# Kernel optimization log

Measured on AMD Instinct MI355X. Metric: run time of the kernel, lower is better.

Reference implementation:

```python
import math
import jax, jax.numpy as jnp
import numpy as np

EMB = 1024
HEADS = 16
HD = EMB // HEADS  # 64
MAXPOS = 1024
BATCH = 4
SEQ = 1024


def get_rope_cache(dim, max_pos, theta=10000.0):
    # NOTE: faithfully reproduces the (i - 1) quirk of the source (not the standard i)
    i = jnp.arange(dim // 2, dtype=jnp.float32)
    theta_i = theta ** (-2.0 * (i - 1.0) / dim)
    pos = jnp.arange(max_pos, dtype=jnp.float32)[:, None]
    th = pos * theta_i  # [max_pos, dim//2]
    return jnp.stack([jnp.cos(th), jnp.sin(th)], axis=-1)  # [max_pos, dim//2, 2]


def apply_rope(x, rope_cache):
    # x: [B, H, S, hd]. Source casts pairs to float16 before the complex multiply,
    # then the complex32*complex64 product promotes back to float32 -> emulate via
    # an fp16 round-trip on x, with the rotation itself done in fp32.
    B, H, S, hd = x.shape
    rc = rope_cache[:S]  # [S, hd//2, 2]
    xp = x.reshape(B, H, S, hd // 2, 2).astype(jnp.float16).astype(jnp.float32)
    a, b = xp[..., 0], xp[..., 1]
    cos, sin = rc[..., 0], rc[..., 1]
    rot = jnp.stack([a * cos - b * sin, a * sin + b * cos], axis=-1)
    return rot.reshape(B, H, S, hd)


def setup_inputs() -> dict:
    key = jax.random.key(0)
    ks = jax.random.split(key, 5)
    std = math.sqrt(2.0 / (EMB + EMB))
    x = jax.random.normal(ks[0], (BATCH, SEQ, EMB), dtype=jnp.float32)
    padding_mask = jnp.ones((BATCH, SEQ), dtype=jnp.float32)
    Wq = jax.random.normal(ks[1], (EMB, EMB), dtype=jnp.float32) * std
    Wk = jax.random.normal(ks[2], (EMB, EMB), dtype=jnp.float32) * std
    Wv = jax.random.normal(ks[3], (EMB, EMB), dtype=jnp.float32) * std
    Wo = jax.random.normal(ks[4], (EMB, EMB), dtype=jnp.float32) * std
    rope_cache = get_rope_cache(HD, MAXPOS)
    return {"x": x, "padding_mask": padding_mask, "Wq": Wq, "Wk": Wk,
            "Wv": Wv, "Wo": Wo, "rope_cache": rope_cache}


def reference(x, padding_mask, Wq, Wk, Wv, Wo, rope_cache):
    B, S, E = x.shape

    def heads(t):  # [B,S,E] -> [B,H,S,hd]
        return t.reshape(B, S, HEADS, HD).transpose(0, 2, 1, 3)

    q = heads(x @ Wq.T)
    k = heads(x @ Wk.T)
    v = heads(x @ Wv.T)
    q = apply_rope(q, rope_cache)
    k = apply_rope(k, rope_cache)

    scores = jnp.einsum('bhqd,bhkd->bhqk', q, k)  # [B,H,S,S]
    causal = jnp.tril(jnp.ones((S, S), jnp.float32))
    mask = (causal[None, :, :] * padding_mask[:, None, :])[:, None]  # [B,1,S,S]
    scores = jnp.where(mask == 0, jnp.float32(-1e9), scores) / math.sqrt(HD)
    weights = jax.nn.softmax(scores, axis=-1)

    out = jnp.einsum('bhqk,bhkd->bhqd', weights, v)  # [B,H,S,hd]
    # Faithful to source: transpose(-2,-1) then .view(B,S,-1) scrambles head_dim/seq
    out = out.transpose(0, 1, 3, 2).reshape(B, S, E)
    return out @ Wo.T
```

## Files before the change

kernel.cpp:

```cpp
#include <hip/hip_runtime.h>

#define SEQ   1024
#define HEADS 16
#define HD    64
#define BATCH 4
#define EMB   1024

typedef __attribute__((ext_vector_type(8))) short  short8;
typedef __attribute__((ext_vector_type(4))) float  floatx4;

__device__ __forceinline__ unsigned short f2bf(float f) {
    unsigned u = __builtin_bit_cast(unsigned, f);
    u += 0x7FFF + ((u >> 16) & 1);
    return (unsigned short)(u >> 16);
}

__device__ __forceinline__ void g2l16(const void* g, void* l) {
    __builtin_amdgcn_global_load_lds((const __attribute__((address_space(1))) unsigned int*)g,
                                     (__attribute__((address_space(3))) unsigned int*)l,
                                     16, 0, 0);
}

__device__ __forceinline__ short8 ldsfrag(const unsigned short* base, int row, int cq) {
    int ch = cq ^ (row & 7);
    return *(const short8*)(base + row * 64 + ch * 8);
}

__global__ __launch_bounds__(256) void cvt_kernel(
    const float* __restrict__ x,  const float* __restrict__ wq,
    const float* __restrict__ wk, const float* __restrict__ wv,
    const float* __restrict__ wo,
    unsigned short* __restrict__ xb, unsigned short* __restrict__ wqkvP,
    unsigned short* __restrict__ woP) {
    int blk = blockIdx.x;
    int tid = threadIdx.x;
    if (blk < 4096) {
        size_t i = (size_t)blk * 1024 + tid * 4;
        float4 v = *(const float4*)(x + i);
        ushort4 o;
        o.x = f2bf(v.x); o.y = f2bf(v.y); o.z = f2bf(v.z); o.w = f2bf(v.w);
        *(ushort4*)(xb + i) = o;
        return;
    }
    int pblk = blk - 4096;
    const float* src; unsigned short* dst; int n0t, kt;
    if (pblk < 384) {
        n0t = pblk >> 4; kt = pblk & 15;
        int which = n0t >> 3;
        src = (which == 0) ? wq : (which == 1) ? wk : wv;
        src += (size_t)(n0t & 7) * 128 * 1024;
        dst = wqkvP + (size_t)pblk * 8192;
    } else {
        int p2 = pblk - 384;
        n0t = p2 >> 4; kt = p2 & 15;
        src = wo + (size_t)n0t * 128 * 1024;
        dst = woP + (size_t)p2 * 8192;
    }
#pragma unroll
    for (int s = 0; s < 4; s++) {
        int w    = tid * 4 + s;
        int ks   = w >> 9, jj = (w >> 6) & 7, lane = w & 63;
        int row  = jj * 16 + (lane & 15);
        int col  = kt * 64 + ks * 32 + (lane >> 4) * 8;
        const float* sp = src + (size_t)row * 1024 + col;
        float4 v0 = *(const float4*)sp;
        float4 v1 = *(const float4*)(sp + 4);
        ushort4 o0, o1;
        o0.x = f2bf(v0.x); o0.y = f2bf(v0.y); o0.z = f2bf(v0.z); o0.w = f2bf(v0.w);
        o1.x = f2bf(v1.x); o1.y = f2bf(v1.y); o1.z = f2bf(v1.z); o1.w = f2bf(v1.w);
        *(ushort4*)(dst + (size_t)w * 8)     = o0;
        *(ushort4*)(dst + (size_t)w * 8 + 4) = o1;
    }
}

__global__ __launch_bounds__(256) void gemm_qkv(
    const unsigned short* __restrict__ A, const unsigned short* __restrict__ Wp,
    unsigned short* __restrict__ outQ, unsigned short* __restrict__ outK,
    unsigned short* __restrict__ outV, const float* __restrict__ rc,
    int M, int N, int K) {
    __shared__ unsigned short As[2][128 * 64];
    const int tid  = threadIdx.x;
    const int lane = tid & 63;
    const int wid  = tid >> 6;
    const int l15  = lane & 15, quad = lane >> 4;
    const int wm   = (wid & 1) * 64, wn = (wid >> 1) * 64;
    const int nbx  = gridDim.x;
    const int cpx  = (nbx * gridDim.y) >> 3;
    const int bid  = blockIdx.y * nbx + blockIdx.x;
    const int virt = (bid & 7) * cpx + (bid >> 3);
    const int n0t  = virt % nbx;
    const int m0   = (virt / nbx) * 128, n0 = n0t * 128;
    const int boff = tid * 16;

    floatx4 acc[4][4] = {};
    const char* Ab = (const char*)A;
    const size_t rstride = (size_t)K * 2;
    const unsigned short* wpb = Wp + ((size_t)(wn >> 4) * 64 + lane) * 8;

    auto stageA = [&](int bufi, int k0) {
#pragma unroll
        for (int c = 0; c < 4; c++) {
            int o = c * 4096 + boff;
            int row = o >> 7;
            int sw  = ((o >> 4) & 7) ^ (row & 7);
            g2l16(Ab + (size_t)(m0 + row) * rstride + (size_t)k0 * 2 + sw * 16,
                  (char*)As[bufi] + o);
        }
    };

    stageA(0, 0);
    __syncthreads();

    int cur = 0;
    for (int k0 = 0; k0 < K; k0 += 64) {
        const int kt = k0 >> 6;
        const unsigned short* wp = wpb + (size_t)(n0t * 16 + kt) * 8192;
        short8 b8[2][4];
#pragma unroll
        for (int ks = 0; ks < 2; ks++)
#pragma unroll
            for (int j = 0; j < 4; j++)
                b8[ks][j] = *(const short8*)(wp + (ks * 512 + j * 64) * 8);
        __builtin_amdgcn_sched_barrier(0);
        if (k0 + 64 < K) stageA(cur ^ 1, k0 + 64);

        const unsigned short* Ac = As[cur];
#pragma unroll
        for (int ks = 0; ks < 2; ks++) {
            short8 a[4];
#pragma unroll
            for (int i = 0; i < 4; i++) a[i] = ldsfrag(Ac, wm + i * 16 + l15, ks * 4 + quad);
#pragma unroll
            for (int i = 0; i < 4; i++)
#pragma unroll
                for (int j = 0; j < 4; j++)
                    acc[i][j] = __builtin_amdgcn_mfma_f32_16x16x32_bf16(a[i], b8[ks][j], acc[i][j], 0, 0, 0);
        }
        asm volatile("s_waitcnt vmcnt(0)" ::: "memory");
        __syncthreads();
        cur ^= 1;
    }

    const int which = n0 >> 10;
#pragma unroll
    for (int i = 0; i < 4; i++) {
#pragma unroll
        for (int r = 0; r < 4; r++) {
            int m = m0 + wm + i * 16 + quad * 4 + r;
            int bb = m >> 10, s = m & 1023;
#pragma unroll
            for (int j = 0; j < 4; j++) {
                int n = n0 + wn + j * 16 + l15;
                float v = acc[i][j][r];
                int nr = n & 1023, h = nr >> 6, d = nr & 63;
                if (which < 2) {
                    float vp = __shfl_xor(v, 1);
                    float2 cs = *(const float2*)&rc[(size_t)s * 64 + (d & ~1)];
                    v = (l15 & 1) ? (vp * cs.y + v * cs.x) : (v * cs.x - vp * cs.y);
                    unsigned short* dst = (which == 0) ? outQ : outK;
                    dst[(((size_t)bb * HEADS + h) * SEQ + s) * HD + d] = f2bf(v);
                } else {
                    outV[(((size_t)bb * HEADS + h) * HD + d) * SEQ + s] = f2bf(v);
                }
            }
        }
    }
}

__global__ __launch_bounds__(256) void gemm_proj64(
    const unsigned short* __restrict__ A, const unsigned short* __restrict__ Wp,
    float* __restrict__ out, int M, int N, int K) {
    __shared__ unsigned short As[2][64 * 64];
    const int tid  = threadIdx.x;
    const int lane = tid & 63;
    const int wid  = tid >> 6;
    const int l15  = lane & 15, quad = lane >> 4;
    const int wm   = (wid & 1) * 32, wn = (wid >> 1) * 64;
    const int n0t  = blockIdx.x;
    const int m0   = blockIdx.y * 64, n0 = n0t * 128;
    const int boff = tid * 16;

    floatx4 acc[2][4] = {};
    const char* Ab = (const char*)A;
    const size_t rstride = (size_t)K * 2;
    const unsigned short* wpb = Wp + ((size_t)(wn >> 4) * 64 + lane) * 8;

    auto stageA = [&](int bufi, int k0) {
#pragma unroll
        for (int c = 0; c < 2; c++) {
            int o = c * 4096 + boff;
            int row = o >> 7;
            int sw  = ((o >> 4) & 7) ^ (row & 7);
            g2l16(Ab + (size_t)(m0 + row) * rstride + (size_t)k0 * 2 + sw * 16,
                  (char*)As[bufi] + o);
        }
    };

    stageA(0, 0);
    __syncthreads();

    int cur = 0;
    for (int k0 = 0; k0 < K; k0 += 64) {
        const int kt = k0 >> 6;
        const unsigned short* wp = wpb + (size_t)(n0t * 16 + kt) * 8192;
        short8 b8[2][4];
#pragma unroll
        for (int ks = 0; ks < 2; ks++)
#pragma unroll
            for (int j = 0; j < 4; j++)
                b8[ks][j] = *(const short8*)(wp + (ks * 512 + j * 64) * 8);
        __builtin_amdgcn_sched_barrier(0);
        if (k0 + 64 < K) stageA(cur ^ 1, k0 + 64);

        const unsigned short* Ac = As[cur];
#pragma unroll
        for (int ks = 0; ks < 2; ks++) {
            short8 a[2];
#pragma unroll
            for (int i = 0; i < 2; i++) a[i] = ldsfrag(Ac, wm + i * 16 + l15, ks * 4 + quad);
#pragma unroll
            for (int i = 0; i < 2; i++)
#pragma unroll
                for (int j = 0; j < 4; j++)
                    acc[i][j] = __builtin_amdgcn_mfma_f32_16x16x32_bf16(a[i], b8[ks][j], acc[i][j], 0, 0, 0);
        }
        asm volatile("s_waitcnt vmcnt(0)" ::: "memory");
        __syncthreads();
        cur ^= 1;
    }

#pragma unroll
    for (int i = 0; i < 2; i++) {
#pragma unroll
        for (int r = 0; r < 4; r++) {
            int m = m0 + wm + i * 16 + quad * 4 + r;
#pragma unroll
            for (int j = 0; j < 4; j++) {
                int n = n0 + wn + j * 16 + l15;
                out[(size_t)m * N + n] = acc[i][j][r];
            }
        }
    }
}

__global__ __launch_bounds__(256) void attn_kernel(
    const unsigned short* __restrict__ Qb, const unsigned short* __restrict__ Kb,
    const unsigned short* __restrict__ VTb, const float* __restrict__ pm,
    unsigned short* __restrict__ Tb) {
    __shared__ unsigned short Ks[2][64 * 64];
    __shared__ unsigned short Vs[2][64 * 64];
    const int tid  = threadIdx.x;
    const int lane = tid & 63, wid = tid >> 6;
    const int l15  = lane & 15, quad = lane >> 4;
    const int bh   = blockIdx.x, b = bh >> 4;
    const int q0   = (15 - blockIdx.y) * 64;
    const int qw   = q0 + wid * 16;
    const int q    = qw + l15;
    const unsigned short* Qh  = Qb  + (size_t)bh * SEQ * HD;
    const unsigned short* Kh  = Kb  + (size_t)bh * SEQ * HD;
    const unsigned short* VTh = VTb + (size_t)bh * HD * SEQ;
    unsigned short*       Th  = Tb  + (size_t)bh * HD * SEQ;
    const float* pmb = pm + b * SEQ;
    const float SCL2 = 0.125f * 1.44269504088896340736f;

    short8 qf0 = *(const short8*)&Qh[(size_t)q * HD + quad * 8];
    short8 qf1 = *(const short8*)&Qh[(size_t)q * HD + 32 + quad * 8];

    floatx4 ot[4] = {};
    float l_lane = 0.f;
    const int boff = tid * 16;
    const int srcA = l15 + ((quad & 1) << 5);
    const int srcB = srcA + 16;
    const bool hi  = (quad >> 1) & 1;

    auto stageKV = [&](int bufi, int kvc) {
        const char* kg = (const char*)(Kh + (size_t)kvc * HD);
        const char* vg = (const char*)(VTh + kvc);
#pragma unroll
        for (int c = 0; c < 2; c++) {
            int o = c * 4096 + boff;
            int row = o >> 7;
            int sw  = ((o >> 4) & 7) ^ (row & 7);
            g2l16(kg + (size_t)row * 128 + sw * 16, (char*)Ks[bufi] + o);
            g2l16(vg + (size_t)row * (SEQ * 2) + sw * 16, (char*)Vs[bufi] + o);
        }
    };

    stageKV(0, 0);
    __syncthreads();

    int cur = 0;
    for (int kvc = 0; kvc <= q0; kvc += 64) {
        if (kvc + 64 <= q0) stageKV(cur ^ 1, kvc + 64);

        const unsigned short* Kc = Ks[cur];
        const unsigned short* Vc = Vs[cur];
        const bool diag = (kvc + 63 > qw);
        floatx4 sc[4];
#pragma unroll
        for (int st = 0; st < 4; st++) {
            short8 ka0 = ldsfrag(Kc, st * 16 + l15, quad);
            short8 ka1 = ldsfrag(Kc, st * 16 + l15, 4 + quad);
            floatx4 z = {0.f, 0.f, 0.f, 0.f};
            z = __builtin_amdgcn_mfma_f32_16x16x32_bf16(ka0, qf0, z, 0, 0, 0);
            z = __builtin_amdgcn_mfma_f32_16x16x32_bf16(ka1, qf1, z, 0, 0, 0);
            sc[st] = z;
        }
        unsigned w0[4], w1[4];
#pragma unroll
        for (int st = 0; st < 4; st++) {
            int kvbase = kvc + st * 16 + quad * 4;
            float4 pmv = *(const float4*)&pmb[kvbase];
            float p[4];
#pragma unroll
            for (int r = 0; r < 4; r++) {
                float e = exp2f(sc[st][r] * SCL2) * (((&pmv.x)[r] != 0.f) ? 1.f : 0.f);
                if (diag && (kvbase + r > q)) e = 0.f;
                l_lane += e;
                p[r] = e;
            }
            w0[st] = (unsigned)f2bf(p[0]) | ((unsigned)f2bf(p[1]) << 16);
            w1[st] = (unsigned)f2bf(p[2]) | ((unsigned)f2bf(p[3]) << 16);
        }
        unsigned a0 = __shfl(w0[0], srcA), a1 = __shfl(w0[1], srcA);
        unsigned b0 = __shfl(w1[0], srcA), b1 = __shfl(w1[1], srcA);
        unsigned c0 = __shfl(w0[0], srcB), c1 = __shfl(w0[1], srcB);
        unsigned d0 = __shfl(w1[0], srcB), d1 = __shfl(w1[1], srcB);
        uint4 f0 = { hi ? a1 : a0, hi ? b1 : b0, hi ? c1 : c0, hi ? d1 : d0 };
        short8 pf0 = __builtin_bit_cast(short8, f0);
        a0 = __shfl(w0[2], srcA); a1 = __shfl(w0[3], srcA);
        b0 = __shfl(w1[2], srcA); b1 = __shfl(w1[3], srcA);
        c0 = __shfl(w0[2], srcB); c1 = __shfl(w0[3], srcB);
        d0 = __shfl(w1[2], srcB); d1 = __shfl(w1[3], srcB);
        uint4 f1 = { hi ? a1 : a0, hi ? b1 : b0, hi ? c1 : c0, hi ? d1 : d0 };
        short8 pf1 = __builtin_bit_cast(short8, f1);

#pragma unroll
        for (int jt = 0; jt < 4; jt++) {
            short8 v0 = ldsfrag(Vc, jt * 16 + l15, quad);
            short8 v1 = ldsfrag(Vc, jt * 16 + l15, 4 + quad);
            ot[jt] = __builtin_amdgcn_mfma_f32_16x16x32_bf16(v0, pf0, ot[jt], 0, 0, 0);
            ot[jt] = __builtin_amdgcn_mfma_f32_16x16x32_bf16(v1, pf1, ot[jt], 0, 0, 0);
        }

        asm volatile("s_waitcnt vmcnt(0)" ::: "memory");
        __syncthreads();
        cur ^= 1;
    }

    float l = l_lane;
    l += __shfl_xor(l, 16);
    l += __shfl_xor(l, 32);
    float inv = 1.0f / l;
#pragma unroll
    for (int jt = 0; jt < 4; jt++)
#pragma unroll
        for (int r = 0; r < 4; r++)
            Th[(size_t)(jt * 16 + quad * 4 + r) * SEQ + q] = f2bf(ot[jt][r] * inv);
}

extern "C" void kernel_launch(void* const* d_in, const int* in_sizes, int n_in,
                              void* d_out, int out_size, void* d_ws, size_t ws_size,
                              hipStream_t stream) {
    const float* x  = (const float*)d_in[0];
    const float* pm = (const float*)d_in[1];
    const float* Wq = (const float*)d_in[2];
    const float* Wk = (const float*)d_in[3];
    const float* Wv = (const float*)d_in[4];
    const float* Wo = (const float*)d_in[5];
    const float* rc = (const float*)d_in[6];

    char* base = (char*)d_ws;
    unsigned short* xb    = (unsigned short*)(base);
    unsigned short* wqkvP = (unsigned short*)(base + (8u  << 20));
    unsigned short* woP   = (unsigned short*)(base + (14u << 20));
    unsigned short* Qb    = (unsigned short*)(base + (16u << 20));
    unsigned short* Kb    = (unsigned short*)(base + (24u << 20));
    unsigned short* VTb   = (unsigned short*)(base + (32u << 20));
    unsigned short* Tb    = (unsigned short*)(base + (40u << 20));

    cvt_kernel<<<4608, 256, 0, stream>>>(x, Wq, Wk, Wv, Wo, xb, wqkvP, woP);
    gemm_qkv<<<dim3(24, 32), 256, 0, stream>>>(xb, wqkvP, Qb, Kb, VTb,
                                               rc, 4096, 3072, 1024);
    attn_kernel<<<dim3(64, 16), 256, 0, stream>>>(Qb, Kb, VTb, pm, Tb);
    gemm_proj64<<<dim3(8, 64), 256, 0, stream>>>(Tb, woP, (float*)d_out, 4096, 1024, 1024);
}
```

Before: 194.1 us.

## Software-pipeline QKV GEMM B-fragment loads and stage Wo through LDS

The QKV GEMM loop is unrolled by two with ping-pong registers for the packed weight fragments, so the next tile's B loads and A staging are issued before the current MFMAs. Partial vmcnt waits replace the full drain. The output projection stops using the pre-packed fragment layout: Wo is converted to plain row-major bf16 and streamed into a second swizzled LDS buffer alongside A. This trades the packing work and direct global fragment loads for more LDS traffic and shared-memory use. The cvt grid grows to cover Wo as a flat elementwise conversion.

```diff
diff --git a/kernel.cpp b/kernel.cpp
--- a/kernel.cpp
+++ b/kernel.cpp
@@ -31,7 +31,7 @@
     const float* __restrict__ wk, const float* __restrict__ wv,
     const float* __restrict__ wo,
     unsigned short* __restrict__ xb, unsigned short* __restrict__ wqkvP,
-    unsigned short* __restrict__ woP) {
+    unsigned short* __restrict__ wob) {
     int blk = blockIdx.x;
     int tid = threadIdx.x;
     if (blk < 4096) {
@@ -42,35 +42,36 @@
         *(ushort4*)(xb + i) = o;
         return;
     }
-    int pblk = blk - 4096;
-    const float* src; unsigned short* dst; int n0t, kt;
-    if (pblk < 384) {
-        n0t = pblk >> 4; kt = pblk & 15;
+    if (blk < 4480) {
+        int pblk = blk - 4096;
+        int n0t = pblk >> 4, kt = pblk & 15;
         int which = n0t >> 3;
-        src = (which == 0) ? wq : (which == 1) ? wk : wv;
+        const float* src = (which == 0) ? wq : (which == 1) ? wk : wv;
         src += (size_t)(n0t & 7) * 128 * 1024;
-        dst = wqkvP + (size_t)pblk * 8192;
-    } else {
-        int p2 = pblk - 384;
-        n0t = p2 >> 4; kt = p2 & 15;
-        src = wo + (size_t)n0t * 128 * 1024;
-        dst = woP + (size_t)p2 * 8192;
-    }
-#pragma unroll
-    for (int s = 0; s < 4; s++) {
-        int w    = tid * 4 + s;
-        int ks   = w >> 9, jj = (w >> 6) & 7, lane = w & 63;
-        int row  = jj * 16 + (lane & 15);
-        int col  = kt * 64 + ks * 32 + (lane >> 4) * 8;
-        const float* sp = src + (size_t)row * 1024 + col;
-        float4 v0 = *(const float4*)sp;
-        float4 v1 = *(const float4*)(sp + 4);
-        ushort4 o0, o1;
-        o0.x = f2bf(v0.x); o0.y = f2bf(v0.y); o0.z = f2bf(v0.z); o0.w = f2bf(v0.w);
-        o1.x = f2bf(v1.x); o1.y = f2bf(v1.y); o1.z = f2bf(v1.z); o1.w = f2bf(v1.w);
-        *(ushort4*)(dst + (size_t)w * 8)     = o0;
-        *(ushort4*)(dst + (size_t)w * 8 + 4) = o1;
-    }
+        unsigned short* dst = wqkvP + (size_t)pblk * 8192;
+#pragma unroll
+        for (int s = 0; s < 4; s++) {
+            int w    = tid * 4 + s;
+            int ks   = w >> 9, jj = (w >> 6) & 7, lane = w & 63;
+            int row  = jj * 16 + (lane & 15);
+            int col  = kt * 64 + ks * 32 + (lane >> 4) * 8;
+            const float* sp = src + (size_t)row * 1024 + col;
+            float4 v0 = *(const float4*)sp;
+            float4 v1 = *(const float4*)(sp + 4);
+            ushort4 o0, o1;
+            o0.x = f2bf(v0.x); o0.y = f2bf(v0.y); o0.z = f2bf(v0.z); o0.w = f2bf(v0.w);
+            o1.x = f2bf(v1.x); o1.y = f2bf(v1.y); o1.z = f2bf(v1.z); o1.w = f2bf(v1.w);
+            *(ushort4*)(dst + (size_t)w * 8)     = o0;
+            *(ushort4*)(dst + (size_t)w * 8 + 4) = o1;
+        }
+        return;
+    }
+    int rel = blk - 4480;
+    size_t i = (size_t)rel * 1024 + tid * 4;
+    float4 v = *(const float4*)(wo + i);
+    ushort4 o;
+    o.x = f2bf(v.x); o.y = f2bf(v.y); o.z = f2bf(v.z); o.w = f2bf(v.w);
+    *(ushort4*)(wob + i) = o;
 }
 
 __global__ __launch_bounds__(256) void gemm_qkv(
@@ -97,34 +98,25 @@
     const size_t rstride = (size_t)K * 2;
     const unsigned short* wpb = Wp + ((size_t)(wn >> 4) * 64 + lane) * 8;
 
-    auto stageA = [&](int bufi, int k0) {
+    auto stageA = [&](int bufi, int kt) {
 #pragma unroll
         for (int c = 0; c < 4; c++) {
             int o = c * 4096 + boff;
             int row = o >> 7;
             int sw  = ((o >> 4) & 7) ^ (row & 7);
-            g2l16(Ab + (size_t)(m0 + row) * rstride + (size_t)k0 * 2 + sw * 16,
+            g2l16(Ab + (size_t)(m0 + row) * rstride + (size_t)(kt << 6) * 2 + sw * 16,
                   (char*)As[bufi] + o);
         }
     };
-
-    stageA(0, 0);
-    __syncthreads();
-
-    int cur = 0;
-    for (int k0 = 0; k0 < K; k0 += 64) {
-        const int kt = k0 >> 6;
+    auto loadB = [&](short8 (&b)[2][4], int kt) {
         const unsigned short* wp = wpb + (size_t)(n0t * 16 + kt) * 8192;
-        short8 b8[2][4];
 #pragma unroll
         for (int ks = 0; ks < 2; ks++)
 #pragma unroll
             for (int j = 0; j < 4; j++)
-                b8[ks][j] = *(const short8*)(wp + (ks * 512 + j * 64) * 8);
-        __builtin_amdgcn_sched_barrier(0);
-        if (k0 + 64 < K) stageA(cur ^ 1, k0 + 64);
-
-        const unsigned short* Ac = As[cur];
+                b[ks][j] = *(const short8*)(wp + (ks * 512 + j * 64) * 8);
+    };
+    auto mfmaStep = [&](const unsigned short* Ac, short8 (&b)[2][4]) {
 #pragma unroll
         for (int ks = 0; ks < 2; ks++) {
             short8 a[4];
@@ -134,11 +126,32 @@
             for (int i = 0; i < 4; i++)
 #pragma unroll
                 for (int j = 0; j < 4; j++)
-                    acc[i][j] = __builtin_amdgcn_mfma_f32_16x16x32_bf16(a[i], b8[ks][j], acc[i][j], 0, 0, 0);
-        }
-        asm volatile("s_waitcnt vmcnt(0)" ::: "memory");
-        __syncthreads();
-        cur ^= 1;
+                    acc[i][j] = __builtin_amdgcn_mfma_f32_16x16x32_bf16(a[i], b[ks][j], acc[i][j], 0, 0, 0);
+        }
+    };
+
+    short8 bA[2][4], bB[2][4];
+    stageA(0, 0);
+    loadB(bA, 0);
+    asm volatile("s_waitcnt vmcnt(8)" ::: "memory");
+    __builtin_amdgcn_sched_barrier(0);
+    __builtin_amdgcn_s_barrier();
+
+    for (int kt = 0; kt < 16; kt += 2) {
+        if (kt + 1 < 16) { stageA(1, kt + 1); loadB(bB, kt + 1); }
+        __builtin_amdgcn_sched_barrier(0);
+        mfmaStep(As[0], bA);
+        asm volatile("s_waitcnt vmcnt(8) lgkmcnt(0)" ::: "memory");
+        __builtin_amdgcn_sched_barrier(0);
+        __builtin_amdgcn_s_barrier();
+        if (kt + 2 < 16) { stageA(0, kt + 2); loadB(bA, kt + 2); }
+        __builtin_amdgcn_sched_barrier(0);
+        mfmaStep(As[1], bB);
+        if (kt + 2 < 16) {
+            asm volatile("s_waitcnt vmcnt(8) lgkmcnt(0)" ::: "memory");
+            __builtin_amdgcn_sched_barrier(0);
+            __builtin_amdgcn_s_barrier();
+        }
     }
 
     const int which = n0 >> 10;
@@ -168,24 +181,24 @@
 }
 
 __global__ __launch_bounds__(256) void gemm_proj64(
-    const unsigned short* __restrict__ A, const unsigned short* __restrict__ Wp,
+    const unsigned short* __restrict__ A, const unsigned short* __restrict__ W,
     float* __restrict__ out, int M, int N, int K) {
     __shared__ unsigned short As[2][64 * 64];
+    __shared__ unsigned short Bs[2][128 * 64];
     const int tid  = threadIdx.x;
     const int lane = tid & 63;
     const int wid  = tid >> 6;
     const int l15  = lane & 15, quad = lane >> 4;
     const int wm   = (wid & 1) * 32, wn = (wid >> 1) * 64;
-    const int n0t  = blockIdx.x;
-    const int m0   = blockIdx.y * 64, n0 = n0t * 128;
+    const int m0   = blockIdx.y * 64, n0 = blockIdx.x * 128;
     const int boff = tid * 16;
 
     floatx4 acc[2][4] = {};
     const char* Ab = (const char*)A;
+    const char* Wb = (const char*)W;
     const size_t rstride = (size_t)K * 2;
-    const unsigned short* wpb = Wp + ((size_t)(wn >> 4) * 64 + lane) * 8;
-
-    auto stageA = [&](int bufi, int k0) {
+
+    auto stageStep = [&](int bufi, int k0) {
 #pragma unroll
         for (int c = 0; c < 2; c++) {
             int o = c * 4096 + boff;
@@ -194,36 +207,39 @@
             g2l16(Ab + (size_t)(m0 + row) * rstride + (size_t)k0 * 2 + sw * 16,
                   (char*)As[bufi] + o);
         }
+#pragma unroll
+        for (int c = 0; c < 4; c++) {
+            int o = c * 4096 + boff;
+            int row = o >> 7;
+            int sw  = ((o >> 4) & 7) ^ (row & 7);
+            g2l16(Wb + (size_t)(n0 + row) * rstride + (size_t)k0 * 2 + sw * 16,
+                  (char*)Bs[bufi] + o);
+        }
     };
 
-    stageA(0, 0);
+    stageStep(0, 0);
     __syncthreads();
 
     int cur = 0;
     for (int k0 = 0; k0 < K; k0 += 64) {
-        const int kt = k0 >> 6;
-        const unsigned short* wp = wpb + (size_t)(n0t * 16 + kt) * 8192;
-        short8 b8[2][4];
-#pragma unroll
-        for (int ks = 0; ks < 2; ks++)
-#pragma unroll
-            for (int j = 0; j < 4; j++)
-                b8[ks][j] = *(const short8*)(wp + (ks * 512 + j * 64) * 8);
-        __builtin_amdgcn_sched_barrier(0);
-        if (k0 + 64 < K) stageA(cur ^ 1, k0 + 64);
+        if (k0 + 64 < K) stageStep(cur ^ 1, k0 + 64);
 
         const unsigned short* Ac = As[cur];
+        const unsigned short* Bc = Bs[cur];
 #pragma unroll
         for (int ks = 0; ks < 2; ks++) {
-            short8 a[2];
+            short8 a[2], b[4];
 #pragma unroll
             for (int i = 0; i < 2; i++) a[i] = ldsfrag(Ac, wm + i * 16 + l15, ks * 4 + quad);
 #pragma unroll
+            for (int j = 0; j < 4; j++) b[j] = ldsfrag(Bc, wn + j * 16 + l15, ks * 4 + quad);
+#pragma unroll
             for (int i = 0; i < 2; i++)
 #pragma unroll
                 for (int j = 0; j < 4; j++)
-                    acc[i][j] = __builtin_amdgcn_mfma_f32_16x16x32_bf16(a[i], b8[ks][j], acc[i][j], 0, 0, 0);
-        }
+                    acc[i][j] = __builtin_amdgcn_mfma_f32_16x16x32_bf16(a[i], b[j], acc[i][j], 0, 0, 0);
+        }
+
         asm volatile("s_waitcnt vmcnt(0)" ::: "memory");
         __syncthreads();
         cur ^= 1;
@@ -373,15 +389,15 @@
     char* base = (char*)d_ws;
     unsigned short* xb    = (unsigned short*)(base);
     unsigned short* wqkvP = (unsigned short*)(base + (8u  << 20));
-    unsigned short* woP   = (unsigned short*)(base + (14u << 20));
+    unsigned short* wob   = (unsigned short*)(base + (14u << 20));
     unsigned short* Qb    = (unsigned short*)(base + (16u << 20));
     unsigned short* Kb    = (unsigned short*)(base + (24u << 20));
     unsigned short* VTb   = (unsigned short*)(base + (32u << 20));
     unsigned short* Tb    = (unsigned short*)(base + (40u << 20));
 
-    cvt_kernel<<<4608, 256, 0, stream>>>(x, Wq, Wk, Wv, Wo, xb, wqkvP, woP);
+    cvt_kernel<<<5504, 256, 0, stream>>>(x, Wq, Wk, Wv, Wo, xb, wqkvP, wob);
     gemm_qkv<<<dim3(24, 32), 256, 0, stream>>>(xb, wqkvP, Qb, Kb, VTb,
                                                rc, 4096, 3072, 1024);
     attn_kernel<<<dim3(64, 16), 256, 0, stream>>>(Qb, Kb, VTb, pm, Tb);
-    gemm_proj64<<<dim3(8, 64), 256, 0, stream>>>(Tb, woP, (float*)d_out, 4096, 1024, 1024);
-}
+    gemm_proj64<<<dim3(8, 64), 256, 0, stream>>>(Tb, wob, (float*)d_out, 4096, 1024, 1024);
+}
```

Result: no change. 196.7 us (+1.4%).
